# Optimization experiments

Measured on AMD Instinct MI355X. Metric: run time of the kernel, lower is better.

The kernel has to match this reference:

```python
import jax, jax.numpy as jnp
import numpy as np

D_MODEL = 512
N_HEAD = 8
D_HEAD = 64
N_LAYER = 4
D_INNER = 2048
IN_CH = 2048
N_CLS = 64
B, T = 2, 2048
LN_EPS = 1e-5


def layer_norm(x, s, b):
    mu = jnp.mean(x, axis=-1, keepdims=True)
    var = jnp.mean(jnp.square(x - mu), axis=-1, keepdims=True)
    return (x - mu) * jax.lax.rsqrt(var + LN_EPS) * s + b


def rel_shift(x):
    # x: [q, k, b, n] -> Transformer-XL relative shift
    q, k, b, n = x.shape
    zp = jnp.zeros((q, 1, b, n), x.dtype)
    x = jnp.concatenate([zp, x], axis=1)          # [q, k+1, b, n]
    x = x.reshape(k + 1, q, b, n)[1:]             # drop first row
    return x.reshape(q, k, b, n)


def setup_inputs() -> dict:
    key = jax.random.key(0)
    ks = jax.random.split(key, 12)
    s = 0.02
    return {
        "x": jax.random.normal(ks[0], (B, IN_CH, T), jnp.float32),
        "emb_w": jax.random.normal(ks[1], (D_MODEL, IN_CH), jnp.float32) * s,
        "emb_b": jnp.zeros((D_MODEL,), jnp.float32),
        "r_w_bias": jax.random.normal(ks[2], (N_HEAD, D_HEAD), jnp.float32) * s,
        "r_r_bias": jax.random.normal(ks[3], (N_HEAD, D_HEAD), jnp.float32) * s,
        "qkv_w": jax.random.normal(ks[4], (N_LAYER, 3 * N_HEAD * D_HEAD, D_MODEL), jnp.float32) * s,
        "qkv_b": jnp.zeros((N_LAYER, 3 * N_HEAD * D_HEAD), jnp.float32),
        "r_proj_w": jax.random.normal(ks[5], (N_LAYER, N_HEAD * D_HEAD, D_MODEL), jnp.float32) * s,
        "o_w": jax.random.normal(ks[6], (N_LAYER, D_MODEL, N_HEAD * D_HEAD), jnp.float32) * s,
        "ln1_s": jnp.ones((N_LAYER, D_MODEL), jnp.float32),
        "ln1_b": jnp.zeros((N_LAYER, D_MODEL), jnp.float32),
        "ff1_w": jax.random.normal(ks[7], (N_LAYER, D_INNER, D_MODEL), jnp.float32) * s,
        "ff1_b": jnp.zeros((N_LAYER, D_INNER), jnp.float32),
        "ff2_w": jax.random.normal(ks[8], (N_LAYER, D_MODEL, D_INNER), jnp.float32) * s,
        "ff2_b": jnp.zeros((N_LAYER, D_MODEL), jnp.float32),
        "ln2_s": jnp.ones((N_LAYER, D_MODEL), jnp.float32),
        "ln2_b": jnp.zeros((N_LAYER, D_MODEL), jnp.float32),
        "cls_w": jax.random.normal(ks[9], (N_CLS, D_MODEL), jnp.float32) * s,
        "cls_b": jnp.zeros((N_CLS,), jnp.float32),
    }


def reference(x, emb_w, emb_b, r_w_bias, r_r_bias, qkv_w, qkv_b, r_proj_w, o_w,
              ln1_s, ln1_b, ff1_w, ff1_b, ff2_w, ff2_b, ln2_s, ln2_b, cls_w, cls_b):
    b, _, t = x.shape
    d = D_MODEL
    # 1x1 conv embedding, then to [T, B, d_model] layout as in _forward
    h = jnp.einsum('dc,bct->tbd', emb_w, x) + emb_b

    # sinusoidal positional embedding over pos_seq = klen-1 .. 0 (klen == qlen, mem_len=0)
    pos_seq = jnp.arange(t - 1, -1, -1, dtype=h.dtype)
    inv_freq = 1.0 / (10000.0 ** (jnp.arange(0, d, 2, dtype=h.dtype) / d))
    sinusoid = pos_seq[:, None] * inv_freq[None, :]
    pos_emb = jnp.concatenate([jnp.sin(sinusoid), jnp.cos(sinusoid)], axis=-1)  # [T, d]

    scale = 1.0 / (D_HEAD ** 0.5)
    for i in range(N_LAYER):
        w = h
        heads = jnp.einsum('ed,tbd->tbe', qkv_w[i], w) + qkv_b[i]          # [T,B,3*H*Dh]
        q, k, v = jnp.split(heads, 3, axis=-1)
        q = q.reshape(t, b, N_HEAD, D_HEAD)
        k = k.reshape(t, b, N_HEAD, D_HEAD)
        v = v.reshape(t, b, N_HEAD, D_HEAD)
        r_head_k = jnp.einsum('ed,td->te', r_proj_w[i], pos_emb).reshape(t, N_HEAD, D_HEAD)

        AC = jnp.einsum('ibnd,jbnd->ijbn', q + r_w_bias, k)                # content term
        BD = rel_shift(jnp.einsum('ibnd,jnd->ijbn', q + r_r_bias, r_head_k))  # position term
        attn_prob = jax.nn.softmax((AC + BD) * scale, axis=1)              # softmax over keys
        attn_vec = jnp.einsum('ijbn,jbnd->ibnd', attn_prob, v).reshape(t, b, N_HEAD * D_HEAD)
        attn_out = jnp.einsum('de,tbe->tbd', o_w[i], attn_vec)             # o_net (no bias)
        h = layer_norm(w + attn_out, ln1_s[i], ln1_b[i])                   # post-lnorm

        ff = jnp.einsum('fd,tbd->tbf', ff1_w[i], h) + ff1_b[i]
        ff = jax.nn.relu(ff)
        ff = jnp.einsum('df,tbf->tbd', ff2_w[i], ff) + ff2_b[i]
        h = layer_norm(h + ff, ln2_s[i], ln2_b[i])

    # 1x1 conv classifier -> [B, num_classes, T]
    out = jnp.einsum('kd,tbd->bkt', cls_w, h) + cls_b[None, :, None]
    return out
```

## Files before the change

### kernel.cpp

```cpp
#include <hip/hip_runtime.h>
#include <hip/hip_bf16.h>
#include <math.h>


#define T_   2048
#define B_   2
#define DM   512
#define NH   8
#define DH   64
#define DI   2048
#define INCH 2048
#define NCLS 64
#define MT   4096

typedef __attribute__((ext_vector_type(8))) short short8;
typedef __attribute__((ext_vector_type(4))) float float4v;

#define QSCALE 0.1803368801111204f

__device__ inline ushort f2bf(float f) {
  uint u = __float_as_uint(f);
  return (ushort)((u + 0x7FFFu + ((u >> 16) & 1u)) >> 16);
}
__device__ inline float bf2f(ushort h) { return __uint_as_float(((uint)h) << 16); }
__device__ inline uint pkbf(float a, float b) {
  __hip_bfloat162 h = __float22bfloat162_rn(float2{a, b});
  return *(uint*)&h;
}
__device__ inline void gload16(const void* g, void* lds) {
  __builtin_amdgcn_global_load_lds(
      (const __attribute__((address_space(1))) void*)g,
      (__attribute__((address_space(3))) void*)lds, 16, 0, 0);
}

__global__ __launch_bounds__(256) void pos_kernel(ushort* __restrict__ pe) {
  int idx = blockIdx.x * 256 + threadIdx.x;
  if (idx >= T_ * DM) return;
  int t = idx >> 9;
  int i = idx & 511;
  int j = (i < 256) ? i : (i - 256);
  double invf = exp(-(double)(2 * j) * (9.210340371976184 / 512.0));
  double a = (double)(T_ - 1 - t) * invf;
  pe[idx] = f2bf((i < 256) ? (float)sin(a) : (float)cos(a));
}

__global__ __launch_bounds__(256) void cvt6_kernel(
    const float* s0, ushort* d0, int n0,
    const float* s1, ushort* d1, int n1,
    const float* s2, ushort* d2, int n2,
    const float* s3, ushort* d3, int n3,
    const float* s4, ushort* d4, int n4,
    const float* s5, ushort* d5, int n5)
{
  const float* s; ushort* d; int n;
  switch (blockIdx.y) {
    case 0: s = s0; d = d0; n = n0; break;
    case 1: s = s1; d = d1; n = n1; break;
    case 2: s = s2; d = d2; n = n2; break;
    case 3: s = s3; d = d3; n = n3; break;
    case 4: s = s4; d = d4; n = n4; break;
    default: s = s5; d = d5; n = n5; break;
  }
  int i = blockIdx.x * 256 + threadIdx.x;
  if (i >= n) return;
  float4 v = ((const float4*)s)[i];
  ushort4 w = { f2bf(v.x), f2bf(v.y), f2bf(v.z), f2bf(v.w) };
  ((ushort4*)d)[i] = w;
}

__global__ __launch_bounds__(256) void xpose_kernel(const float* __restrict__ x,
                                                    ushort* __restrict__ xb) {
  __shared__ float s[32][33];
  int t0 = blockIdx.x * 32, k0 = blockIdx.y * 32, b = blockIdx.z;
  int tx = threadIdx.x & 31, ty = threadIdx.x >> 5;
#pragma unroll
  for (int l = 0; l < 4; ++l) {
    int k = k0 + ty + l * 8;
    s[ty + l * 8][tx] = x[((size_t)b * INCH + k) * T_ + t0 + tx];
  }
  __syncthreads();
#pragma unroll
  for (int l = 0; l < 4; ++l) {
    int t = t0 + ty + l * 8;
    xb[((size_t)(t * 2 + b)) * INCH + k0 + tx] = f2bf(s[tx][ty + l * 8]);
  }
}

__global__ __launch_bounds__(256) void vtrans_kernel(const ushort* __restrict__ heads,
                                                     ushort* __restrict__ vtg) {
  __shared__ ushort s[64][72];
  const int tid = threadIdx.x;
  int t0 = blockIdx.x * 64;
  int b = blockIdx.y & 1, n = blockIdx.y >> 1;
  for (int e = tid; e < 512; e += 256) {
    int r = e >> 3, c = e & 7;
    *(uint4*)&s[r][c * 8] =
        *(const uint4*)&heads[(size_t)((t0 + r) * 2 + b) * 1536 + 1024 + n * 64 + c * 8];
  }
  __syncthreads();
  for (int e = tid; e < 512; e += 256) {
    int d = e >> 3, c = e & 7;
    ushort tmp[8];
#pragma unroll
    for (int j = 0; j < 8; ++j) tmp[j] = s[c * 8 + j][d];
    *(uint4*)&vtg[((size_t)((b * 8 + n) * 64 + d)) * (size_t)T_ + t0 + c * 8] = *(uint4*)tmp;
  }
}

template<int TM, int OUTMODE, bool RELU>
__global__ __launch_bounds__(256) void gemm_bf16(
    const ushort* __restrict__ A, const ushort* __restrict__ W,
    const float* __restrict__ bias, float* __restrict__ Cf, ushort* __restrict__ Cb,
    int M, int N, int K)
{
  __shared__ __attribute__((aligned(16))) ushort As[TM * 64];
  __shared__ __attribute__((aligned(16))) ushort Bs[128 * 64];
  const int NI = TM / 32;
  const int tid  = threadIdx.x;
  const int wave = tid >> 6, lane = tid & 63;
  const int quad = lane >> 4, lidx = lane & 15;
  const int m0 = blockIdx.y * TM, n0 = blockIdx.x * 128;
  const int r8 = lane >> 3;
  const int cs = ((lane & 7) ^ (r8 & 7)) * 8;

  float4v acc[NI * 4];
#pragma unroll
  for (int i = 0; i < NI * 4; ++i) acc[i] = (float4v){0.f, 0.f, 0.f, 0.f};

  const int wm = (wave >> 1) * (TM / 2), wn = (wave & 1) * 64;

  for (int k0 = 0; k0 < K; k0 += 64) {
    __syncthreads();
#pragma unroll
    for (int g = 0; g < TM / 32; ++g) {
      int r0 = wave * 8 + g * 32;
      gload16(A + (size_t)(m0 + r0 + r8) * K + k0 + cs, &As[r0 * 64]);
    }
#pragma unroll
    for (int g = 0; g < 4; ++g) {
      int r0 = wave * 8 + g * 32;
      gload16(W + (size_t)(n0 + r0 + r8) * K + k0 + cs, &Bs[r0 * 64]);
    }
    __syncthreads();

#pragma unroll
    for (int kb = 0; kb < 2; ++kb) {
      short8 af[NI], bf4[4];
      const int ch = (((kb * 4 + quad) ^ (lidx & 7)) * 8);
#pragma unroll
      for (int i = 0; i < NI; ++i)
        af[i] = *(const short8*)&As[(wm + i * 16 + lidx) * 64 + ch];
#pragma unroll
      for (int j = 0; j < 4; ++j)
        bf4[j] = *(const short8*)&Bs[(wn + j * 16 + lidx) * 64 + ch];
#pragma unroll
      for (int i = 0; i < NI; ++i)
#pragma unroll
        for (int j = 0; j < 4; ++j)
          acc[i * 4 + j] = __builtin_amdgcn_mfma_f32_16x16x32_bf16(af[i], bf4[j], acc[i * 4 + j], 0, 0, 0);
    }
  }

  float bj[4];
#pragma unroll
  for (int j = 0; j < 4; ++j) bj[j] = bias ? bias[n0 + wn + j * 16 + lidx] : 0.f;
#pragma unroll
  for (int i = 0; i < NI; ++i) {
    int rbase = m0 + wm + i * 16 + quad * 4;
#pragma unroll
    for (int j = 0; j < 4; ++j) {
      int col = n0 + wn + j * 16 + lidx;
#pragma unroll
      for (int reg = 0; reg < 4; ++reg) {
        float v = acc[i * 4 + j][reg] + bj[j];
        if (RELU) v = fmaxf(v, 0.f);
        size_t off = (size_t)(rbase + reg) * N + col;
        if (OUTMODE != 1) Cf[off] = v;
        if (OUTMODE != 0) Cb[off] = f2bf(v);
      }
    }
  }
}

#define BM 128
#define BN 128
#define BK 16
#define LDT 132

__global__ __launch_bounds__(256) void gemm_f32(
    const float* __restrict__ A, const float* __restrict__ W,
    const float* __restrict__ bias, float* __restrict__ C,
    int M, int N, int K)
{
  __shared__ float Asm[BK][LDT];
  __shared__ float Wsm[BK][LDT];
  const int tid = threadIdx.x;
  const int m0 = blockIdx.y * BM;
  const int n0 = blockIdx.x * BN;
  const int row = tid >> 1;
  const int kh  = (tid & 1) * 8;
  const int ty  = tid >> 4;
  const int tx  = tid & 15;

  float acc[8][8];
#pragma unroll
  for (int i = 0; i < 8; ++i)
#pragma unroll
    for (int j = 0; j < 8; ++j) acc[i][j] = 0.f;

  for (int kt = 0; kt < K; kt += BK) {
    float a_reg[8], w_reg[8];
    {
      const float* ap = A + (size_t)(m0 + row) * K + (kt + kh);
      float4 v0 = *(const float4*)ap;
      float4 v1 = *(const float4*)(ap + 4);
      a_reg[0] = v0.x; a_reg[1] = v0.y; a_reg[2] = v0.z; a_reg[3] = v0.w;
      a_reg[4] = v1.x; a_reg[5] = v1.y; a_reg[6] = v1.z; a_reg[7] = v1.w;
    }
    {
      int nn = n0 + row;
      if (nn < N) {
        const float* wp = W + (size_t)nn * K + (kt + kh);
        float4 v0 = *(const float4*)wp;
        float4 v1 = *(const float4*)(wp + 4);
        w_reg[0] = v0.x; w_reg[1] = v0.y; w_reg[2] = v0.z; w_reg[3] = v0.w;
        w_reg[4] = v1.x; w_reg[5] = v1.y; w_reg[6] = v1.z; w_reg[7] = v1.w;
      } else {
#pragma unroll
        for (int q = 0; q < 8; ++q) w_reg[q] = 0.f;
      }
    }
    __syncthreads();
#pragma unroll
    for (int q = 0; q < 8; ++q) { Asm[kh + q][row] = a_reg[q]; Wsm[kh + q][row] = w_reg[q]; }
    __syncthreads();
#pragma unroll
    for (int k = 0; k < BK; ++k) {
      float4 a0 = *(const float4*)&Asm[k][ty * 4];
      float4 a1 = *(const float4*)&Asm[k][ty * 4 + 64];
      float4 b0 = *(const float4*)&Wsm[k][tx * 4];
      float4 b1 = *(const float4*)&Wsm[k][tx * 4 + 64];
      float av[8] = {a0.x, a0.y, a0.z, a0.w, a1.x, a1.y, a1.z, a1.w};
      float bv[8] = {b0.x, b0.y, b0.z, b0.w, b1.x, b1.y, b1.z, b1.w};
#pragma unroll
      for (int i = 0; i < 8; ++i)
#pragma unroll
        for (int j = 0; j < 8; ++j) acc[i][j] += av[i] * bv[j];
    }
  }

#pragma unroll
  for (int ih = 0; ih < 2; ++ih)
#pragma unroll
    for (int i = 0; i < 4; ++i) {
      int m = m0 + ty * 4 + ih * 64 + i;
#pragma unroll
      for (int jh = 0; jh < 2; ++jh) {
        int nn = n0 + tx * 4 + jh * 64;
        if (nn < N) {
          float4 v;
          v.x = acc[ih * 4 + i][jh * 4 + 0] + bias[nn + 0];
          v.y = acc[ih * 4 + i][jh * 4 + 1] + bias[nn + 1];
          v.z = acc[ih * 4 + i][jh * 4 + 2] + bias[nn + 2];
          v.w = acc[ih * 4 + i][jh * 4 + 3] + bias[nn + 3];
          *(float4*)&C[(size_t)m * N + nn] = v;
        }
      }
    }
}

#define GT 68

__device__ inline short8 bfrag(const char* base, int lidx, int quad, int kb) {
  return *(const short8*)(base + lidx * 128 + ((((kb << 2) + quad) ^ (lidx & 7)) << 4));
}

__global__ __launch_bounds__(256, 3) void attn_mfma_kernel(
    const ushort* __restrict__ heads, const ushort* __restrict__ rk,
    const ushort* __restrict__ vtg,
    const float* __restrict__ rwb, const float* __restrict__ rrb,
    float* __restrict__ Oacc, float* __restrict__ Lg)
{
  __shared__ __attribute__((aligned(16))) ushort Ks[64 * 64];
  __shared__ __attribute__((aligned(16))) ushort Vt[64 * 64];
  __shared__ __attribute__((aligned(16))) ushort Re[128 * 64];
  __shared__ __attribute__((aligned(16))) ushort Gbt[128 * GT];

  const int tid  = threadIdx.x;
  const int i0   = blockIdx.x * 64;
  const int b    = blockIdx.y & 1;
  const int n    = blockIdx.y >> 1;
  const int chunk = blockIdx.z;
  const int jt0 = (chunk == 0) ? 0  : (chunk == 1 ? 11 : 22);
  const int jt1 = (chunk == 0) ? 11 : (chunk == 1 ? 22 : 32);
  const int wave = tid >> 6;
  const int lane = tid & 63;
  const int quad = lane >> 4;
  const int lidx = lane & 15;
  const int r8   = lane >> 3;
  const int cs8  = ((lane & 7) ^ (r8 & 7)) * 8;
  const int bn64 = (b * 8 + n) * 64;
  const int rloc = wave * 16 + lidx;

  short8 qw[2], qr4[4][2], q4[2];
  {
    auto qfrag = [&](int row, int kb, const float* bias) -> short8 {
      short8 q;
      if (row < T_) q = *(const short8*)&heads[(size_t)(row * 2 + b) * 1536 + n * 64 + kb * 32 + quad * 8];
      else { for (int t = 0; t < 8; ++t) ((ushort*)&q)[t] = 0; }
      short8 o;
#pragma unroll
      for (int t = 0; t < 8; ++t) {
        float f = (bf2f((ushort)((ushort*)&q)[t]) + bias[n * 64 + kb * 32 + quad * 8 + t]) * QSCALE;
        ((ushort*)&o)[t] = f2bf(f);
      }
      return o;
    };
    qw[0] = qfrag(i0 + rloc, 0, rwb);
    qw[1] = qfrag(i0 + rloc, 1, rwb);
#pragma unroll
    for (int rt = 0; rt < 4; ++rt) {
      int row = i0 + rt * 16 + lidx;
      qr4[rt][0] = qfrag(row, 0, rrb); qr4[rt][1] = qfrag(row, 1, rrb);
    }
    int row4 = i0 + 64 + lidx;
    q4[0] = qfrag(row4, 0, rrb); q4[1] = qfrag(row4, 1, rrb);
  }

  int a0[4];
#pragma unroll
  for (int t = 0; t < 4; ++t)
    a0[t] = (t * 16 + quad * 4 + 63 - rloc) * GT + rloc;

  float4v oacc[4];
  float4v liacc = (float4v){0.f, 0.f, 0.f, 0.f};
#pragma unroll
  for (int dt = 0; dt < 4; ++dt) oacc[dt] = (float4v){0.f, 0.f, 0.f, 0.f};
  short8 ones8;
#pragma unroll
  for (int t = 0; t < 8; ++t) ((ushort*)&ones8)[t] = 0x3F80;

  auto stageKRe = [&](int jt) {
    int j0 = jt * 64, qmin = j0 + 1984 - i0;
#pragma unroll
    for (int half = 0; half < 2; ++half) {
      int r0 = 8 * wave + 32 * half;
      gload16(heads + (size_t)((j0 + r0 + r8) * 2 + b) * 1536 + 512 + n * 64 + cs8, &Ks[r0 * 64]);
    }
#pragma unroll
    for (int q4i = 0; q4i < 4; ++q4i) {
      int r0 = 8 * wave + 32 * q4i;
      int qh = qmin + r0 + r8;
      int p  = (qh > T_) ? (qh - T_ - 1) : ((qh == T_) ? 0 : qh);
      gload16(rk + (size_t)p * 2048 + n * 64 + cs8, &Re[r0 * 64]);
    }
  };
  auto stageV = [&](int jt) {
    int j0 = jt * 64;
#pragma unroll
    for (int half = 0; half < 2; ++half) {
      int r0 = 8 * wave + 32 * half;
      gload16(vtg + (size_t)(bn64 + r0 + r8) * (size_t)T_ + j0 + cs8, &Vt[r0 * 64]);
    }
  };
  auto fixup = [&](int jt) {
    int qmin = jt * 64 + 1984 - i0;
    int Tidx = T_ - qmin;
    if (Tidx >= 0 && Tidx < 128) {
      if (tid < 32) ((uint*)Re)[Tidx * 32 + tid] = 0u;
      __syncthreads();
    }
  };

  stageKRe(jt0);
  stageV(jt0);
  __syncthreads();
  fixup(jt0);

  for (int jt = jt0; jt < jt1; ++jt) {
    const int qmin = jt * 64 + 1984 - i0;
    const int wth  = T_ - qmin;

    float4v sv[4];
#pragma unroll
    for (int t = 0; t < 4; ++t) {
      const char* KsT = (const char*)Ks + t * 2048;
      short8 kf0 = bfrag(KsT, lidx, quad, 0);
      short8 kf1 = bfrag(KsT, lidx, quad, 1);
      float4v c = {0.f, 0.f, 0.f, 0.f};
      c = __builtin_amdgcn_mfma_f32_16x16x32_bf16(kf0, qw[0], c, 0, 0, 0);
      c = __builtin_amdgcn_mfma_f32_16x16x32_bf16(kf1, qw[1], c, 0, 0, 0);
      sv[t] = c;
    }

#pragma unroll
    for (int si = 0; si < 2; ++si) {
      const int ws = wave + si * 4;
      const int w0 = ws * 16;
      const char* ReW = (const char*)Re + w0 * 128;
      short8 rb0 = bfrag(ReW, lidx, quad, 0);
      short8 rb1 = bfrag(ReW, lidx, quad, 1);
#pragma unroll
      for (int rt = 0; rt < 4; ++rt) {
        bool need = si == 0 ? (rt >= 3 - wave) : (rt <= 3 - wave);
        if (need) {
          float4v g = {0.f, 0.f, 0.f, 0.f};
          g = __builtin_amdgcn_mfma_f32_16x16x32_bf16(qr4[rt][0], rb0, g, 0, 0, 0);
          g = __builtin_amdgcn_mfma_f32_16x16x32_bf16(qr4[rt][1], rb1, g, 0, 0, 0);
          uint2 st; st.x = pkbf(g[0], g[1]); st.y = pkbf(g[2], g[3]);
          *(uint2*)&Gbt[(w0 + lidx) * GT + rt * 16 + quad * 4] = st;
        }
      }
      if (si == 0 && wth < 63) {
        float4v g = {0.f, 0.f, 0.f, 0.f};
        g = __builtin_amdgcn_mfma_f32_16x16x32_bf16(q4[0], rb0, g, 0, 0, 0);
        g = __builtin_amdgcn_mfma_f32_16x16x32_bf16(q4[1], rb1, g, 0, 0, 0);
        if (quad == 0) Gbt[(w0 + lidx) * GT + 64] = f2bf(g[0]);
      }
    }
    __syncthreads();

    if (jt + 1 < jt1) stageKRe(jt + 1);

    {
      const int cth = wth + rloc - 63;
#pragma unroll
      for (int t = 0; t < 4; ++t) {
        const int c0 = t * 16 + quad * 4;
#pragma unroll
        for (int r = 0; r < 4; ++r) {
          int ga = a0[t] + r * GT + ((c0 + r > cth) ? 1 : 0);
          sv[t][r] = __builtin_amdgcn_exp2f(sv[t][r] + bf2f(Gbt[ga]));
        }
      }
    }

    short8 vb[4][2];
#pragma unroll
    for (int dt = 0; dt < 4; ++dt) {
      const char* VtT = (const char*)Vt + dt * 2048;
      vb[dt][0] = bfrag(VtT, lidx, quad, 0);
      vb[dt][1] = bfrag(VtT, lidx, quad, 1);
    }

    short8 af[2];
#pragma unroll
    for (int kb = 0; kb < 2; ++kb) {
      uint mm[4];
#pragma unroll
      for (int i = 0; i < 2; ++i) {
        uint e, o;
        asm("v_cvt_pk_bf16_f32 %0, %1, %2" : "=v"(e) : "v"(sv[2 * kb][2 * i]),     "v"(sv[2 * kb][2 * i + 1]));
        asm("v_cvt_pk_bf16_f32 %0, %1, %2" : "=v"(o) : "v"(sv[2 * kb + 1][2 * i]), "v"(sv[2 * kb + 1][2 * i + 1]));
        asm("v_permlane32_swap_b32 %0, %1" : "+v"(e), "+v"(o));
        asm("v_permlane16_swap_b32 %0, %1" : "+v"(e), "+v"(o));
        mm[i] = e; mm[2 + i] = o;
      }
      union { uint u[4]; short8 s; } cv;
      cv.u[0] = mm[0]; cv.u[1] = mm[1]; cv.u[2] = mm[2]; cv.u[3] = mm[3];
      af[kb] = cv.s;
    }

    __syncthreads();

    if (jt + 1 < jt1) {
      stageV(jt + 1);
      fixup(jt + 1);
    }

#pragma unroll
    for (int dt = 0; dt < 4; ++dt) {
      oacc[dt] = __builtin_amdgcn_mfma_f32_16x16x32_bf16(af[0], vb[dt][0], oacc[dt], 0, 0, 0);
      oacc[dt] = __builtin_amdgcn_mfma_f32_16x16x32_bf16(af[1], vb[dt][1], oacc[dt], 0, 0, 0);
    }
    liacc = __builtin_amdgcn_mfma_f32_16x16x32_bf16(af[0], ones8, liacc, 0, 0, 0);
    liacc = __builtin_amdgcn_mfma_f32_16x16x32_bf16(af[1], ones8, liacc, 0, 0, 0);
  }

  const int rowg0 = (b * 8 + n) * T_ + i0 + wave * 16 + quad * 4;
#pragma unroll
  for (int reg = 0; reg < 4; ++reg) {
    int rowg = rowg0 + reg;
#pragma unroll
    for (int dt = 0; dt < 4; ++dt)
      atomicAdd(&Oacc[(size_t)rowg * 64 + dt * 16 + lidx], oacc[dt][reg]);
    if (lidx == 0) atomicAdd(&Lg[rowg], liacc[reg]);
  }
}

__global__ __launch_bounds__(256) void zero2_kernel(float4* __restrict__ a, int na,
                                                    float4* __restrict__ b2, int nb) {
  int i = blockIdx.x * 256 + threadIdx.x;
  if (i < na) a[i] = float4{0.f, 0.f, 0.f, 0.f};
  int j = i - na;
  if (j >= 0 && j < nb) b2[j] = float4{0.f, 0.f, 0.f, 0.f};
}

__global__ __launch_bounds__(256) void attn_norm_kernel(const float* __restrict__ Oacc,
                                                        const float* __restrict__ Lg,
                                                        ushort* __restrict__ avec) {
  int idx = blockIdx.x * 256 + threadIdx.x;
  int d4  = idx & 15;
  int row = (idx >> 4) & 2047;
  int bn  = idx >> 15;
  float4 v = ((const float4*)Oacc)[idx];
  float inv = 1.0f / Lg[(bn << 11) + row];
  int b = bn >> 3, n = bn & 7;
  ushort4 w = { f2bf(v.x * inv), f2bf(v.y * inv), f2bf(v.z * inv), f2bf(v.w * inv) };
  *(ushort4*)&avec[(size_t)(row * 2 + b) * DM + n * 64 + d4 * 4] = w;
}

__global__ __launch_bounds__(256) void ln_res_kernel(
    float* __restrict__ h, ushort* __restrict__ hb, const float* __restrict__ delta,
    const float* __restrict__ s, const float* __restrict__ bb)
{
  const int m = blockIdx.x;
  const int tid = threadIdx.x;
  float* hp = h + (size_t)m * DM;
  ushort* hbp = hb + (size_t)m * DM;
  const float* dp = delta + (size_t)m * DM;
  float x0 = hp[tid] + dp[tid];
  float x1 = hp[tid + 256] + dp[tid + 256];
  float sum = x0 + x1, sq = x0 * x0 + x1 * x1;
#pragma unroll
  for (int o = 32; o > 0; o >>= 1) { sum += __shfl_down(sum, o); sq += __shfl_down(sq, o); }
  __shared__ float part[8];
  int wv = tid >> 6;
  if ((tid & 63) == 0) { part[wv * 2] = sum; part[wv * 2 + 1] = sq; }
  __syncthreads();
  float ts = part[0] + part[2] + part[4] + part[6];
  float tq = part[1] + part[3] + part[5] + part[7];
  float mu = ts * (1.f / DM);
  float var = tq * (1.f / DM) - mu * mu;
  float rs = rsqrtf(var + 1e-5f);
  float y0 = (x0 - mu) * rs * s[tid]       + bb[tid];
  float y1 = (x1 - mu) * rs * s[tid + 256] + bb[tid + 256];
  hp[tid] = y0;       hbp[tid] = f2bf(y0);
  hp[tid + 256] = y1; hbp[tid + 256] = f2bf(y1);
}

__global__ __launch_bounds__(256) void reorder_kernel(const float* __restrict__ ct,
                                                      float* __restrict__ out) {
  int idx = blockIdx.x * 256 + threadIdx.x;
  if (idx >= B_ * NCLS * T_) return;
  int t  = idx & (T_ - 1);
  int nc = (idx >> 11) & 63;
  int bb = idx >> 17;
  out[idx] = ct[(size_t)(t * B_ + bb) * NCLS + nc];
}

extern "C" void kernel_launch(void* const* d_in, const int* in_sizes, int n_in,
                              void* d_out, int out_size, void* d_ws, size_t ws_size,
                              hipStream_t stream)
{
  const float* x     = (const float*)d_in[0];
  const float* emb_w = (const float*)d_in[1];
  const float* emb_b = (const float*)d_in[2];
  const float* rwb   = (const float*)d_in[3];
  const float* rrb   = (const float*)d_in[4];
  const float* qkv_w = (const float*)d_in[5];
  const float* qkv_b = (const float*)d_in[6];
  const float* rproj = (const float*)d_in[7];
  const float* o_w   = (const float*)d_in[8];
  const float* ln1s  = (const float*)d_in[9];
  const float* ln1b  = (const float*)d_in[10];
  const float* ff1w  = (const float*)d_in[11];
  const float* ff1b  = (const float*)d_in[12];
  const float* ff2w  = (const float*)d_in[13];
  const float* ff2b  = (const float*)d_in[14];
  const float* ln2s  = (const float*)d_in[15];
  const float* ln2b  = (const float*)d_in[16];
  const float* clsw  = (const float*)d_in[17];
  const float* clsb  = (const float*)d_in[18];
  float* out = (float*)d_out;

  char* p = (char*)d_ws;
  float*  h       = (float*)p;   p += (size_t)MT * DM * 4;
  float*  tmpf    = (float*)p;   p += (size_t)MT * DM * 4;
  ushort* hb      = (ushort*)p;  p += (size_t)MT * DM * 2;
  ushort* headsb  = (ushort*)p;  p += (size_t)MT * 1536 * 2;
  ushort* peb     = (ushort*)p;  p += (size_t)T_ * DM * 2;
  ushort* rk_all  = (ushort*)p;  p += (size_t)T_ * 2048 * 2;
  ushort* avecb   = (ushort*)p;  p += (size_t)MT * DM * 2;
  ushort* xfb     = (ushort*)p;  p += (size_t)MT * INCH * 2;
  ushort* emb_wb  = (ushort*)p;  p += (size_t)DM * INCH * 2;
  ushort* qkv_wb  = (ushort*)p;  p += (size_t)4 * 1536 * DM * 2;
  ushort* rproj_wb= (ushort*)p;  p += (size_t)4 * DM * DM * 2;
  ushort* o_wb    = (ushort*)p;  p += (size_t)4 * DM * DM * 2;
  ushort* ff1_wb  = (ushort*)p;  p += (size_t)4 * DI * DM * 2;
  ushort* ff2_wb  = (ushort*)p;  p += (size_t)4 * DM * DI * 2;
  float*  Lg      = (float*)p;   p += (size_t)16 * T_ * 4;
  ushort* vtg     = xfb;

  cvt6_kernel<<<dim3(4096, 6), 256, 0, stream>>>(
      emb_w, emb_wb, DM * INCH / 4,
      qkv_w, qkv_wb, 4 * 1536 * DM / 4,
      rproj, rproj_wb, 4 * DM * DM / 4,
      o_w,   o_wb,   4 * DM * DM / 4,
      ff1w,  ff1_wb, 4 * DI * DM / 4,
      ff2w,  ff2_wb, 4 * DM * DI / 4);
  pos_kernel<<<(T_ * DM) / 256, 256, 0, stream>>>(peb);
  xpose_kernel<<<dim3(T_ / 32, INCH / 32, B_), 256, 0, stream>>>(x, xfb);

  gemm_bf16<64, 2, false><<<dim3(DM / 128, MT / 64), 256, 0, stream>>>(
      xfb, emb_wb, emb_b, h, hb, MT, DM, INCH);
  gemm_bf16<128, 1, false><<<dim3(2048 / 128, T_ / 128), 256, 0, stream>>>(
      peb, rproj_wb, nullptr, nullptr, rk_all, T_, 2048, DM);

  const int NO4 = MT * DM / 4;
  const int NL4 = 16 * T_ / 4;

  for (int l = 0; l < 4; ++l) {
    gemm_bf16<128, 1, false><<<dim3(1536 / 128, MT / 128), 256, 0, stream>>>(
        hb, qkv_wb + (size_t)l * 1536 * DM, qkv_b + l * 1536, nullptr, headsb, MT, 1536, DM);
    vtrans_kernel<<<dim3(T_ / 64, B_ * NH), 256, 0, stream>>>(headsb, vtg);
    zero2_kernel<<<(NO4 + NL4 + 255) / 256, 256, 0, stream>>>(
        (float4*)tmpf, NO4, (float4*)Lg, NL4);
    attn_mfma_kernel<<<dim3(T_ / 64, B_ * NH, 3), 256, 0, stream>>>(
        headsb, rk_all + (size_t)l * 512, vtg, rwb, rrb, tmpf, Lg);
    attn_norm_kernel<<<(16 * T_ * 16) / 256, 256, 0, stream>>>(tmpf, Lg, avecb);
    gemm_bf16<32, 0, false><<<dim3(DM / 128, MT / 32), 256, 0, stream>>>(
        avecb, o_wb + (size_t)l * DM * DM, nullptr, tmpf, nullptr, MT, DM, DM);
    ln_res_kernel<<<MT, 256, 0, stream>>>(h, hb, tmpf, ln1s + l * DM, ln1b + l * DM);
    gemm_bf16<128, 1, true><<<dim3(DI / 128, MT / 128), 256, 0, stream>>>(
        hb, ff1_wb + (size_t)l * DI * DM, ff1b + l * DI, nullptr, xfb, MT, DI, DM);
    gemm_bf16<32, 0, false><<<dim3(DM / 128, MT / 32), 256, 0, stream>>>(
        xfb, ff2_wb + (size_t)l * DM * DI, ff2b + l * DM, tmpf, nullptr, MT, DM, DI);
    ln_res_kernel<<<MT, 256, 0, stream>>>(h, hb, tmpf, ln2s + l * DM, ln2b + l * DM);
  }

  gemm_f32<<<dim3(1, MT / BM), 256, 0, stream>>>(h, clsw, clsb, tmpf, MT, NCLS, DM);
  reorder_kernel<<<(B_ * NCLS * T_) / 256, 256, 0, stream>>>(tmpf, out);
}
```

Baseline: 944.5 us.

## Replace attention atomics with per-chunk partial buffers and specialize rel-shift gather

Each of the three key-range chunks in the attention kernel now writes its partial output and row-sum to its own buffer with plain stores instead of atomicAdd. The normalization kernel sums the three partials, so the per-layer zeroing kernel goes away. The rel-shift gather in the exp step also gets fast paths for tiles that are entirely on one side of the shift diagonal, which avoids the per-element compare. In exchange the normalization kernel reads three times as much data, and the code needs extra workspace, part of it aliased into xfb after the V-transpose region.

```diff
diff --git a/kernel.cpp b/kernel.cpp
--- a/kernel.cpp
+++ b/kernel.cpp
@@ -279,7 +279,8 @@
     const ushort* __restrict__ heads, const ushort* __restrict__ rk,
     const ushort* __restrict__ vtg,
     const float* __restrict__ rwb, const float* __restrict__ rrb,
-    float* __restrict__ Oacc, float* __restrict__ Lg)
+    float* __restrict__ O0, float* __restrict__ O1, float* __restrict__ O2,
+    float* __restrict__ Lp)
 {
   __shared__ __attribute__((aligned(16))) ushort Ks[64 * 64];
   __shared__ __attribute__((aligned(16))) ushort Vt[64 * 64];
@@ -422,7 +423,19 @@
 
     if (jt + 1 < jt1) stageKRe(jt + 1);
 
-    {
+    if (wth >= 126) {
+#pragma unroll
+      for (int t = 0; t < 4; ++t)
+#pragma unroll
+        for (int r = 0; r < 4; ++r)
+          sv[t][r] = __builtin_amdgcn_exp2f(sv[t][r] + bf2f(Gbt[a0[t] + r * GT]));
+    } else if (wth < 0) {
+#pragma unroll
+      for (int t = 0; t < 4; ++t)
+#pragma unroll
+        for (int r = 0; r < 4; ++r)
+          sv[t][r] = __builtin_amdgcn_exp2f(sv[t][r] + bf2f(Gbt[a0[t] + r * GT + 1]));
+    } else {
       const int cth = wth + rloc - 63;
 #pragma unroll
       for (int t = 0; t < 4; ++t) {
@@ -477,36 +490,37 @@
     liacc = __builtin_amdgcn_mfma_f32_16x16x32_bf16(af[1], ones8, liacc, 0, 0, 0);
   }
 
+  float* __restrict__ Oc = (chunk == 0) ? O0 : (chunk == 1 ? O1 : O2);
+  float* __restrict__ Lc = Lp + chunk * (16 * T_);
   const int rowg0 = (b * 8 + n) * T_ + i0 + wave * 16 + quad * 4;
 #pragma unroll
   for (int reg = 0; reg < 4; ++reg) {
     int rowg = rowg0 + reg;
 #pragma unroll
     for (int dt = 0; dt < 4; ++dt)
-      atomicAdd(&Oacc[(size_t)rowg * 64 + dt * 16 + lidx], oacc[dt][reg]);
-    if (lidx == 0) atomicAdd(&Lg[rowg], liacc[reg]);
-  }
-}
-
-__global__ __launch_bounds__(256) void zero2_kernel(float4* __restrict__ a, int na,
-                                                    float4* __restrict__ b2, int nb) {
-  int i = blockIdx.x * 256 + threadIdx.x;
-  if (i < na) a[i] = float4{0.f, 0.f, 0.f, 0.f};
-  int j = i - na;
-  if (j >= 0 && j < nb) b2[j] = float4{0.f, 0.f, 0.f, 0.f};
-}
-
-__global__ __launch_bounds__(256) void attn_norm_kernel(const float* __restrict__ Oacc,
-                                                        const float* __restrict__ Lg,
-                                                        ushort* __restrict__ avec) {
+      Oc[(size_t)rowg * 64 + dt * 16 + lidx] = oacc[dt][reg];
+    if (lidx == 0) Lc[rowg] = liacc[reg];
+  }
+}
+
+__global__ __launch_bounds__(256) void attn_norm_kernel(
+    const float* __restrict__ O0, const float* __restrict__ O1,
+    const float* __restrict__ O2, const float* __restrict__ Lp,
+    ushort* __restrict__ avec)
+{
   int idx = blockIdx.x * 256 + threadIdx.x;
   int d4  = idx & 15;
   int row = (idx >> 4) & 2047;
   int bn  = idx >> 15;
-  float4 v = ((const float4*)Oacc)[idx];
-  float inv = 1.0f / Lg[(bn << 11) + row];
+  float4 v0 = ((const float4*)O0)[idx];
+  float4 v1 = ((const float4*)O1)[idx];
+  float4 v2 = ((const float4*)O2)[idx];
+  int rg = (bn << 11) + row;
+  float li = Lp[rg] + Lp[rg + 16 * T_] + Lp[rg + 32 * T_];
+  float inv = 1.0f / li;
   int b = bn >> 3, n = bn & 7;
-  ushort4 w = { f2bf(v.x * inv), f2bf(v.y * inv), f2bf(v.z * inv), f2bf(v.w * inv) };
+  ushort4 w = { f2bf((v0.x + v1.x + v2.x) * inv), f2bf((v0.y + v1.y + v2.y) * inv),
+                f2bf((v0.z + v1.z + v2.z) * inv), f2bf((v0.w + v1.w + v2.w) * inv) };
   *(ushort4*)&avec[(size_t)(row * 2 + b) * DM + n * 64 + d4 * 4] = w;
 }
 
@@ -589,8 +603,11 @@
   ushort* o_wb    = (ushort*)p;  p += (size_t)4 * DM * DM * 2;
   ushort* ff1_wb  = (ushort*)p;  p += (size_t)4 * DI * DM * 2;
   ushort* ff2_wb  = (ushort*)p;  p += (size_t)4 * DM * DI * 2;
-  float*  Lg      = (float*)p;   p += (size_t)16 * T_ * 4;
+  float*  P2      = (float*)p;   p += (size_t)MT * DM * 4;
+  float*  Lp      = (float*)p;   p += (size_t)3 * 16 * T_ * 4;
   ushort* vtg     = xfb;
+  float*  P0      = tmpf;
+  float*  P1      = (float*)(xfb + (size_t)16 * 64 * T_);
 
   cvt6_kernel<<<dim3(4096, 6), 256, 0, stream>>>(
       emb_w, emb_wb, DM * INCH / 4,
@@ -607,18 +624,13 @@
   gemm_bf16<128, 1, false><<<dim3(2048 / 128, T_ / 128), 256, 0, stream>>>(
       peb, rproj_wb, nullptr, nullptr, rk_all, T_, 2048, DM);
 
-  const int NO4 = MT * DM / 4;
-  const int NL4 = 16 * T_ / 4;
-
   for (int l = 0; l < 4; ++l) {
     gemm_bf16<128, 1, false><<<dim3(1536 / 128, MT / 128), 256, 0, stream>>>(
         hb, qkv_wb + (size_t)l * 1536 * DM, qkv_b + l * 1536, nullptr, headsb, MT, 1536, DM);
     vtrans_kernel<<<dim3(T_ / 64, B_ * NH), 256, 0, stream>>>(headsb, vtg);
-    zero2_kernel<<<(NO4 + NL4 + 255) / 256, 256, 0, stream>>>(
-        (float4*)tmpf, NO4, (float4*)Lg, NL4);
     attn_mfma_kernel<<<dim3(T_ / 64, B_ * NH, 3), 256, 0, stream>>>(
-        headsb, rk_all + (size_t)l * 512, vtg, rwb, rrb, tmpf, Lg);
-    attn_norm_kernel<<<(16 * T_ * 16) / 256, 256, 0, stream>>>(tmpf, Lg, avecb);
+        headsb, rk_all + (size_t)l * 512, vtg, rwb, rrb, P0, P1, P2, Lp);
+    attn_norm_kernel<<<(16 * T_ * 16) / 256, 256, 0, stream>>>(P0, P1, P2, Lp, avecb);
     gemm_bf16<32, 0, false><<<dim3(DM / 128, MT / 32), 256, 0, stream>>>(
         avecb, o_wb + (size_t)l * DM * DM, nullptr, tmpf, nullptr, MT, DM, DM);
     ln_res_kernel<<<MT, 256, 0, stream>>>(h, hb, tmpf, ln1s + l * DM, ln1b + l * DM);
```

Result: faster. 909.8 us (-3.7%).
